# Kernel tuning notes

Hardware: AMD Instinct MI355X
Metric: run time of the kernel (lower is better)

The kernel has to match this reference:

```python
import jax, jax.numpy as jnp
import numpy as np

THRESHOLD = 0.9
DECAY = 0.6


def setup_inputs() -> dict:
    key = jax.random.key(0)
    k1, k2, k3 = jax.random.split(key, 3)
    T, B, I, H, O = 100, 256, 784, 1024, 10
    # binary-ish spike input (rand fill, thresholded to emulate Poisson spikes)
    x = (jax.random.uniform(k1, (T, B, I)) < 0.3).astype(jnp.float32)
    W1 = 0.01 * jax.random.normal(k2, (I, H), dtype=jnp.float32)
    W2 = 0.01 * jax.random.normal(k3, (H, O), dtype=jnp.float32)
    return {"input_spikes_time": x, "W1": W1, "W2": W2}


def reference(input_spikes_time, W1, W2):
    T, B, _ = input_spikes_time.shape
    H = W1.shape[1]
    O = W2.shape[1]
    dt = input_spikes_time.dtype

    def lif(mem, current):
        # mem = mem*decay + I; spike if mem >= threshold; soft reset
        mem = mem * DECAY + current
        spikes = (mem >= THRESHOLD).astype(dt)
        mem = mem - spikes * THRESHOLD
        return mem, spikes

    def step(carry, x_t):
        mem1, mem2 = carry
        hidden_u = x_t @ W1                 # [B, H]
        mem1, hidden_spikes = lif(mem1, hidden_u)
        output_u = hidden_spikes @ W2       # [B, O]
        mem2, output_spikes = lif(mem2, output_u)
        return (mem1, mem2), (hidden_spikes, output_spikes)

    init = (jnp.zeros((B, H), dt), jnp.zeros((B, O), dt))
    _, (hidden_all, output_all) = jax.lax.scan(step, init, input_spikes_time)
    return hidden_all, output_all
```

## Files before the change

kernel.cpp:

```cpp
#include <hip/hip_runtime.h>
#include <hip/hip_bf16.h>

#define T_STEPS 100
#define BATCH   256
#define IN_DIM  784
#define HID_DIM 1024
#define OUT_DIM 10
#define M_ROWS  (T_STEPS * BATCH)
#define KPAD    800
#define NT      25
#define STG     12288
#define DECAY   0.6f
#define THRESH  0.9f

typedef __attribute__((ext_vector_type(8))) short bf16x8;
typedef __attribute__((ext_vector_type(4))) float f32x4;

#define PACK8(dstp, v0, v1)                                                                        \
    {                                                                                              \
        unsigned int p0 = __builtin_amdgcn_perm(__builtin_bit_cast(unsigned int, (v0).y),          \
                                                __builtin_bit_cast(unsigned int, (v0).x), 0x07060302u); \
        unsigned int p1 = __builtin_amdgcn_perm(__builtin_bit_cast(unsigned int, (v0).w),          \
                                                __builtin_bit_cast(unsigned int, (v0).z), 0x07060302u); \
        unsigned int p2 = __builtin_amdgcn_perm(__builtin_bit_cast(unsigned int, (v1).y),          \
                                                __builtin_bit_cast(unsigned int, (v1).x), 0x07060302u); \
        unsigned int p3 = __builtin_amdgcn_perm(__builtin_bit_cast(unsigned int, (v1).w),          \
                                                __builtin_bit_cast(unsigned int, (v1).z), 0x07060302u); \
        *(uint4*)(dstp) = make_uint4(p0, p1, p2, p3);                                              \
    }

#define GLL(g, l)                                                                                  \
    __builtin_amdgcn_global_load_lds((const __attribute__((address_space(1))) void*)(g),           \
                                     (__attribute__((address_space(3))) void*)(l), 16, 0, 0)

__device__ __forceinline__ void w1_split_body(const float* __restrict__ W1,
                                              unsigned short* __restrict__ Th,
                                              unsigned short* __restrict__ Tl,
                                              int b2, int t,
                                              unsigned short lh[32][33],
                                              unsigned short ll[32][33]) {
    const int nb = (b2 & 31) * 32;
    const int kb = (b2 >> 5) * 32;
    const int ln = t & 31, lk = t >> 5;
    #pragma unroll
    for (int i = 0; i < 4; ++i) {
        const int k = kb + lk + i * 8;
        const float w = (k < IN_DIM) ? W1[(size_t)k * HID_DIM + nb + ln] : 0.f;
        __hip_bfloat16 h = __float2bfloat16(w);
        float hf = __bfloat162float(h);
        __hip_bfloat16 l = __float2bfloat16(w - hf);
        lh[lk + i * 8][ln] = __builtin_bit_cast(unsigned short, h);
        ll[lk + i * 8][ln] = __builtin_bit_cast(unsigned short, l);
    }
    __syncthreads();
    const int o_n = t >> 3;
    const int o_k = (t & 7) * 4;
    ushort4 vh, vl;
    vh.x = lh[o_k + 0][o_n]; vh.y = lh[o_k + 1][o_n];
    vh.z = lh[o_k + 2][o_n]; vh.w = lh[o_k + 3][o_n];
    vl.x = ll[o_k + 0][o_n]; vl.y = ll[o_k + 1][o_n];
    vl.z = ll[o_k + 2][o_n]; vl.w = ll[o_k + 3][o_n];
    *(ushort4*)&Th[(size_t)(nb + o_n) * KPAD + kb + o_k] = vh;
    *(ushort4*)&Tl[(size_t)(nb + o_n) * KPAD + kb + o_k] = vl;
}

__global__ __launch_bounds__(256) void prep(const float* __restrict__ X,
                                            const float* __restrict__ W1,
                                            unsigned short* __restrict__ Xb,
                                            unsigned short* __restrict__ Th,
                                            unsigned short* __restrict__ Tl,
                                            float* __restrict__ outu) {
    __shared__ unsigned short lh[32][33];
    __shared__ unsigned short ll[32][33];
    const int bid = blockIdx.x;
    const int t   = threadIdx.x;

    if (bid < 10000) {
        const int gid = bid * 256 + t;
        const int r   = gid / 100;
        const int c   = gid - r * 100;
        unsigned short* dst = Xb + (size_t)r * KPAD + c * 8;
        if (c < 98) {
            const float* s = X + (size_t)r * IN_DIM + c * 8;
            float4 v0 = *(const float4*)s, v1 = *(const float4*)(s + 4);
            PACK8(dst, v0, v1);
        } else {
            *(uint4*)dst = make_uint4(0u, 0u, 0u, 0u);
        }
    } else if (bid < 10800) {
        w1_split_body(W1, Th, Tl, bid - 10000, t, lh, ll);
    } else {
        float4* p = (float4*)outu;
        p[(bid - 10800) * 256 + t] = make_float4(0.f, 0.f, 0.f, 0.f);
    }
}

__global__ __launch_bounds__(256) void prep_small(const float* __restrict__ W1,
                                                  unsigned short* __restrict__ Th,
                                                  unsigned short* __restrict__ Tl,
                                                  float* __restrict__ outu) {
    __shared__ unsigned short lh[32][33];
    __shared__ unsigned short ll[32][33];
    const int bid = blockIdx.x;
    const int t   = threadIdx.x;
    if (bid < 800) {
        w1_split_body(W1, Th, Tl, bid, t, lh, ll);
    } else {
        float4* p = (float4*)outu;
        p[(bid - 800) * 256 + t] = make_float4(0.f, 0.f, 0.f, 0.f);
    }
}

__global__ __launch_bounds__(256, 3) void gemm1_pipe2(const unsigned short* __restrict__ Xb,
                                                      const unsigned short* __restrict__ Th,
                                                      const unsigned short* __restrict__ Tl,
                                                      float* __restrict__ C) {
    __shared__ unsigned short smem[2 * STG];

    const int tid = threadIdx.x;
    const int bid = blockIdx.x;
    const int xcd = bid & 7;
    const int j_  = bid >> 3;
    const int m0  = (xcd * 25 + (j_ >> 3)) * 128;
    const int n0  = (j_ & 7) * 128;

    const int lane = tid & 63, wv = tid >> 6;
    const int wm   = (wv & 1) * 64, wn = (wv >> 1) * 64;
    const int ml   = lane & 15, quad = lane >> 4;

    const int row  = tid >> 2;
    const int slot = tid & 3;
    const int sOff = (slot ^ ((row >> 1) & 3)) * 8;

    const unsigned short* gA0 = Xb + (size_t)(m0 + row)      * KPAD + sOff;
    const unsigned short* gA1 = Xb + (size_t)(m0 + row + 64) * KPAD + sOff;
    const unsigned short* gH0 = Th + (size_t)(n0 + row)      * KPAD + sOff;
    const unsigned short* gH1 = Th + (size_t)(n0 + row + 64) * KPAD + sOff;
    const unsigned short* gL0 = Tl + (size_t)(n0 + row)      * KPAD + sOff;
    const unsigned short* gL1 = Tl + (size_t)(n0 + row + 64) * KPAD + sOff;

#define STAGE(bf, it)                                                     \
    {                                                                     \
        unsigned short* b_ = smem + (bf) * STG;                           \
        const int k_ = (it) * 32;                                         \
        GLL(gA0 + k_, b_ + tid * 8);                                      \
        GLL(gA1 + k_, b_ + 2048 + tid * 8);                               \
        GLL(gH0 + k_, b_ + 4096 + tid * 8);                               \
        GLL(gH1 + k_, b_ + 6144 + tid * 8);                               \
        GLL(gL0 + k_, b_ + 8192 + tid * 8);                               \
        GLL(gL1 + k_, b_ + 10240 + tid * 8);                              \
    }

    f32x4 acc[4][4];
    #pragma unroll
    for (int i = 0; i < 4; ++i)
        #pragma unroll
        for (int j = 0; j < 4; ++j)
            acc[i][j] = (f32x4){0.f, 0.f, 0.f, 0.f};

    int offA[4], offB[4];
    #pragma unroll
    for (int i = 0; i < 4; ++i) {
        const int m = wm + i * 16 + ml;
        offA[i] = m * 32 + ((quad ^ ((m >> 1) & 3)) * 8);
    }
    #pragma unroll
    for (int j = 0; j < 4; ++j) {
        const int n = wn + j * 16 + ml;
        offB[j] = n * 32 + ((quad ^ ((n >> 1) & 3)) * 8);
    }

    STAGE(0, 0);

    int buf = 0;
    for (int it = 0; it < NT; ++it) {
        asm volatile("s_waitcnt vmcnt(0)" ::: "memory");
        __builtin_amdgcn_s_barrier();
        asm volatile("" ::: "memory");

        if (it + 1 < NT) STAGE(buf ^ 1, it + 1);

        const unsigned short* base = smem + buf * STG;
        bf16x8 af[4], bh[4], bl[4];
        #pragma unroll
        for (int i = 0; i < 4; ++i)
            af[i] = *(const bf16x8*)&base[offA[i]];
        #pragma unroll
        for (int j = 0; j < 4; ++j) {
            bh[j] = *(const bf16x8*)&base[4096 + offB[j]];
            bl[j] = *(const bf16x8*)&base[8192 + offB[j]];
        }

        __builtin_amdgcn_s_setprio(1);
        #pragma unroll
        for (int i = 0; i < 4; ++i)
            #pragma unroll
            for (int j = 0; j < 4; ++j) {
                acc[i][j] = __builtin_amdgcn_mfma_f32_16x16x32_bf16(af[i], bh[j], acc[i][j], 0, 0, 0);
                acc[i][j] = __builtin_amdgcn_mfma_f32_16x16x32_bf16(af[i], bl[j], acc[i][j], 0, 0, 0);
            }
        __builtin_amdgcn_s_setprio(0);

        buf ^= 1;
    }
#undef STAGE

    #pragma unroll
    for (int i = 0; i < 4; ++i)
        #pragma unroll
        for (int j = 0; j < 4; ++j) {
            const int r0 = m0 + wm + i * 16 + quad * 4;
            const int c0 = n0 + wn + j * 16 + ml;
            #pragma unroll
            for (int r = 0; r < 4; ++r)
                C[(size_t)(r0 + r) * HID_DIM + c0] = acc[i][j][r];
        }
}

__global__ __launch_bounds__(256, 3) void gemm1_fallback(const float* __restrict__ X,
                                                         const unsigned short* __restrict__ Th,
                                                         const unsigned short* __restrict__ Tl,
                                                         float* __restrict__ C) {
    __shared__ unsigned short As[128 * 32];
    __shared__ unsigned short Bhs[128 * 32];
    __shared__ unsigned short Bls[128 * 32];

    const int tid = threadIdx.x;
    const int bid = blockIdx.x;
    const int xcd = bid & 7;
    const int j_  = bid >> 3;
    const int m0  = (xcd * 25 + (j_ >> 3)) * 128;
    const int n0  = (j_ & 7) * 128;

    const int lane = tid & 63, wv = tid >> 6;
    const int wm   = (wv & 1) * 64, wn = (wv >> 1) * 64;
    const int ml   = lane & 15, quad = lane >> 4;

    const int sr = tid >> 2;
    const int sc = tid & 3;
    const int f0 = (sr >> 1) & 3;
    const int w0 = sr * 32 + ((sc ^ f0) * 8);
    const int w1 = (sr + 64) * 32 + ((sc ^ f0) * 8);

    const float*          Xa = X  + (size_t)(m0 + sr)      * IN_DIM + sc * 8;
    const float*          Xc = X  + (size_t)(m0 + sr + 64) * IN_DIM + sc * 8;
    const unsigned short* Ha = Th + (size_t)(n0 + sr)      * KPAD   + sc * 8;
    const unsigned short* Hb = Th + (size_t)(n0 + sr + 64) * KPAD   + sc * 8;
    const unsigned short* La = Tl + (size_t)(n0 + sr)      * KPAD   + sc * 8;
    const unsigned short* Lb = Tl + (size_t)(n0 + sr + 64) * KPAD   + sc * 8;

    f32x4 acc[4][4];
    #pragma unroll
    for (int i = 0; i < 4; ++i)
        #pragma unroll
        for (int j = 0; j < 4; ++j)
            acc[i][j] = (f32x4){0.f, 0.f, 0.f, 0.f};

    float4 xa0 = *(const float4*)&Xa[0], xa1 = *(const float4*)&Xa[4];
    float4 xb0 = *(const float4*)&Xc[0], xb1 = *(const float4*)&Xc[4];
    uint4  vh0 = *(const uint4*)&Ha[0],  vh1 = *(const uint4*)&Hb[0];
    uint4  vl0 = *(const uint4*)&La[0],  vl1 = *(const uint4*)&Lb[0];
    PACK8(&As[w0], xa0, xa1);
    PACK8(&As[w1], xb0, xb1);
    *(uint4*)&Bhs[w0] = vh0;  *(uint4*)&Bhs[w1] = vh1;
    *(uint4*)&Bls[w0] = vl0;  *(uint4*)&Bls[w1] = vl1;
    __syncthreads();

    for (int it = 0; it < NT; ++it) {
        bf16x8 af[4], bh[4], bl[4];
        #pragma unroll
        for (int i = 0; i < 4; ++i) {
            const int m = wm + i * 16 + ml;
            af[i] = *(const bf16x8*)&As[m * 32 + ((quad ^ ((m >> 1) & 3)) * 8)];
        }
        #pragma unroll
        for (int j = 0; j < 4; ++j) {
            const int n   = wn + j * 16 + ml;
            const int idx = n * 32 + ((quad ^ ((n >> 1) & 3)) * 8);
            bh[j] = *(const bf16x8*)&Bhs[idx];
            bl[j] = *(const bf16x8*)&Bls[idx];
        }

        const bool have_next = (it + 1 < NT);
        if (have_next) {
            const int kt = (it + 1) * 32;
            const int c0 = kt + sc * 8;
            const bool v0 = (c0 < IN_DIM), v1 = (c0 + 4 < IN_DIM);
            xa0 = v0 ? *(const float4*)&Xa[kt]     : make_float4(0.f, 0.f, 0.f, 0.f);
            xa1 = v1 ? *(const float4*)&Xa[kt + 4] : make_float4(0.f, 0.f, 0.f, 0.f);
            xb0 = v0 ? *(const float4*)&Xc[kt]     : make_float4(0.f, 0.f, 0.f, 0.f);
            xb1 = v1 ? *(const float4*)&Xc[kt + 4] : make_float4(0.f, 0.f, 0.f, 0.f);
            vh0 = *(const uint4*)&Ha[kt];  vh1 = *(const uint4*)&Hb[kt];
            vl0 = *(const uint4*)&La[kt];  vl1 = *(const uint4*)&Lb[kt];
        }

        #pragma unroll
        for (int i = 0; i < 4; ++i)
            #pragma unroll
            for (int j = 0; j < 4; ++j) {
                acc[i][j] = __builtin_amdgcn_mfma_f32_16x16x32_bf16(af[i], bh[j], acc[i][j], 0, 0, 0);
                acc[i][j] = __builtin_amdgcn_mfma_f32_16x16x32_bf16(af[i], bl[j], acc[i][j], 0, 0, 0);
            }

        __syncthreads();
        if (have_next) {
            PACK8(&As[w0], xa0, xa1);
            PACK8(&As[w1], xb0, xb1);
            *(uint4*)&Bhs[w0] = vh0;  *(uint4*)&Bhs[w1] = vh1;
            *(uint4*)&Bls[w0] = vl0;  *(uint4*)&Bls[w1] = vl1;
            __syncthreads();
        }
    }

    #pragma unroll
    for (int i = 0; i < 4; ++i)
        #pragma unroll
        for (int j = 0; j < 4; ++j) {
            const int r0 = m0 + wm + i * 16 + quad * 4;
            const int c0 = n0 + wn + j * 16 + ml;
            #pragma unroll
            for (int r = 0; r < 4; ++r)
                C[(size_t)(r0 + r) * HID_DIM + c0] = acc[i][j][r];
        }
}

__global__ __launch_bounds__(256) void lif1_fused(float* __restrict__ hid,
                                                  const float* __restrict__ W2,
                                                  float* __restrict__ outu) {
    const int idx = blockIdx.x * blockDim.x + threadIdx.x;
    const int stride = BATCH * HID_DIM;
    const int b  = idx >> 10;
    const int h0 = idx & 1023;

    float mem = 0.f;
    float u[10];
    #pragma unroll
    for (int c = 0; c < 10; ++c) u[c] = hid[(size_t)c * stride + idx];

    for (int t = 0; t < T_STEPS; t += 10) {
        float nu[10];
        if (t + 10 < T_STEPS) {
            #pragma unroll
            for (int c = 0; c < 10; ++c) nu[c] = hid[(size_t)(t + 10 + c) * stride + idx];
        }
        #pragma unroll
        for (int c = 0; c < 10; ++c) {
            mem = mem * DECAY + u[c];
            float s = (mem >= THRESH) ? 1.f : 0.f;
            mem -= s * THRESH;
            hid[(size_t)(t + c) * stride + idx] = s;
            if (s != 0.f) {
                float* od = outu + (size_t)(t + c) * (BATCH * OUT_DIM) + b * OUT_DIM;
                const float* w = W2 + (size_t)h0 * OUT_DIM;
                #pragma unroll
                for (int o = 0; o < OUT_DIM; ++o) atomicAdd(&od[o], w[o]);
            }
        }
        #pragma unroll
        for (int c = 0; c < 10; ++c) u[c] = nu[c];
    }
}

__global__ __launch_bounds__(256) void lif2(float* __restrict__ outp) {
    const int n = blockIdx.x * blockDim.x + threadIdx.x;
    const int stride = BATCH * OUT_DIM;
    if (n >= stride) return;
    float mem = 0.f;
    float u[10];
    #pragma unroll
    for (int c = 0; c < 10; ++c) u[c] = outp[(size_t)c * stride + n];
    for (int t = 0; t < T_STEPS; t += 10) {
        float nu[10];
        if (t + 10 < T_STEPS) {
            #pragma unroll
            for (int c = 0; c < 10; ++c) nu[c] = outp[(size_t)(t + 10 + c) * stride + n];
        }
        #pragma unroll
        for (int c = 0; c < 10; ++c) {
            mem = mem * DECAY + u[c];
            float s = (mem >= THRESH) ? 1.f : 0.f;
            mem -= s * THRESH;
            outp[(size_t)(t + c) * stride + n] = s;
        }
        #pragma unroll
        for (int c = 0; c < 10; ++c) u[c] = nu[c];
    }
}

extern "C" void kernel_launch(void* const* d_in, const int* in_sizes, int n_in,
                              void* d_out, int out_size, void* d_ws, size_t ws_size,
                              hipStream_t stream) {
    const float* x  = (const float*)d_in[0];
    const float* W1 = (const float*)d_in[1];
    const float* W2 = (const float*)d_in[2];
    float* out  = (float*)d_out;
    float* hid  = out;
    float* outu = out + (size_t)M_ROWS * HID_DIM;

    unsigned short* Th = (unsigned short*)d_ws;
    unsigned short* Tl = Th + (size_t)HID_DIM * KPAD;
    unsigned short* Xb = Tl + (size_t)HID_DIM * KPAD;

    const size_t ws_needed_big =
        (size_t)2 * HID_DIM * KPAD * sizeof(unsigned short) +
        (size_t)M_ROWS * KPAD * sizeof(unsigned short);

    if (ws_size >= ws_needed_big) {
        prep<<<11050, 256, 0, stream>>>(x, W1, Xb, Th, Tl, outu);
        gemm1_pipe2<<<1600, 256, 0, stream>>>(Xb, Th, Tl, hid);
    } else {
        prep_small<<<1050, 256, 0, stream>>>(W1, Th, Tl, outu);
        gemm1_fallback<<<1600, 256, 0, stream>>>(x, Th, Tl, hid);
    }

    lif1_fused<<<(BATCH * HID_DIM) / 256, 256, 0, stream>>>(hid, W2, outu);

    lif2<<<(BATCH * OUT_DIM + 255) / 256, 256, 0, stream>>>(outu);
}
```

Before: 277.2 us.

## Fuse lif2 into lif1 via last-block counter and coarsen prep X conversion

Removes the separate lif2 kernel launch. The last 10 blocks to finish lif1_fused, found through an atomic completion counter, spin until all blocks are done and then run the output-layer LIF scan. The prep kernel also processes four X chunks per thread, cutting its grid from 11050 to 3550 blocks. The counter lives in the workspace and is reset in prep. The spin-wait depends on every lif1 block eventually completing, which holds because the last 10 blocks only wait after all others have incremented the counter.

```diff
diff --git a/kernel.cpp b/kernel.cpp
--- a/kernel.cpp
+++ b/kernel.cpp
@@ -10,6 +10,7 @@
 #define KPAD    800
 #define NT      25
 #define STG     12288
+#define NBLK1   1024
 #define DECAY   0.6f
 #define THRESH  0.9f
 
@@ -69,36 +70,42 @@
                                             unsigned short* __restrict__ Xb,
                                             unsigned short* __restrict__ Th,
                                             unsigned short* __restrict__ Tl,
-                                            float* __restrict__ outu) {
+                                            float* __restrict__ outu,
+                                            unsigned int* __restrict__ ctr) {
     __shared__ unsigned short lh[32][33];
     __shared__ unsigned short ll[32][33];
     const int bid = blockIdx.x;
     const int t   = threadIdx.x;
 
-    if (bid < 10000) {
-        const int gid = bid * 256 + t;
-        const int r   = gid / 100;
-        const int c   = gid - r * 100;
-        unsigned short* dst = Xb + (size_t)r * KPAD + c * 8;
-        if (c < 98) {
-            const float* s = X + (size_t)r * IN_DIM + c * 8;
-            float4 v0 = *(const float4*)s, v1 = *(const float4*)(s + 4);
-            PACK8(dst, v0, v1);
-        } else {
-            *(uint4*)dst = make_uint4(0u, 0u, 0u, 0u);
-        }
-    } else if (bid < 10800) {
-        w1_split_body(W1, Th, Tl, bid - 10000, t, lh, ll);
+    if (bid < 2500) {
+        #pragma unroll
+        for (int i = 0; i < 4; ++i) {
+            const int gid = (bid * 256 + t) + i * 640000;
+            const int r   = gid / 100;
+            const int c   = gid - r * 100;
+            unsigned short* dst = Xb + (size_t)r * KPAD + c * 8;
+            if (c < 98) {
+                const float* s = X + (size_t)r * IN_DIM + c * 8;
+                float4 v0 = *(const float4*)s, v1 = *(const float4*)(s + 4);
+                PACK8(dst, v0, v1);
+            } else {
+                *(uint4*)dst = make_uint4(0u, 0u, 0u, 0u);
+            }
+        }
+    } else if (bid < 3300) {
+        w1_split_body(W1, Th, Tl, bid - 2500, t, lh, ll);
     } else {
+        if (bid == 3300 && t == 0) *ctr = 0u;
         float4* p = (float4*)outu;
-        p[(bid - 10800) * 256 + t] = make_float4(0.f, 0.f, 0.f, 0.f);
+        p[(bid - 3300) * 256 + t] = make_float4(0.f, 0.f, 0.f, 0.f);
     }
 }
 
 __global__ __launch_bounds__(256) void prep_small(const float* __restrict__ W1,
                                                   unsigned short* __restrict__ Th,
                                                   unsigned short* __restrict__ Tl,
-                                                  float* __restrict__ outu) {
+                                                  float* __restrict__ outu,
+                                                  unsigned int* __restrict__ ctr) {
     __shared__ unsigned short lh[32][33];
     __shared__ unsigned short ll[32][33];
     const int bid = blockIdx.x;
@@ -106,6 +113,7 @@
     if (bid < 800) {
         w1_split_body(W1, Th, Tl, bid, t, lh, ll);
     } else {
+        if (bid == 800 && t == 0) *ctr = 0u;
         float4* p = (float4*)outu;
         p[(bid - 800) * 256 + t] = make_float4(0.f, 0.f, 0.f, 0.f);
     }
@@ -326,7 +334,8 @@
 
 __global__ __launch_bounds__(256) void lif1_fused(float* __restrict__ hid,
                                                   const float* __restrict__ W2,
-                                                  float* __restrict__ outu) {
+                                                  float* __restrict__ outu,
+                                                  unsigned int* __restrict__ ctr) {
     const int idx = blockIdx.x * blockDim.x + threadIdx.x;
     const int stride = BATCH * HID_DIM;
     const int b  = idx >> 10;
@@ -359,31 +368,42 @@
         #pragma unroll
         for (int c = 0; c < 10; ++c) u[c] = nu[c];
     }
-}
-
-__global__ __launch_bounds__(256) void lif2(float* __restrict__ outp) {
-    const int n = blockIdx.x * blockDim.x + threadIdx.x;
-    const int stride = BATCH * OUT_DIM;
-    if (n >= stride) return;
-    float mem = 0.f;
-    float u[10];
-    #pragma unroll
-    for (int c = 0; c < 10; ++c) u[c] = outp[(size_t)c * stride + n];
+
+    __shared__ unsigned int s_old;
+    __threadfence();
+    __syncthreads();
+    if (threadIdx.x == 0) s_old = atomicAdd(ctr, 1u);
+    __syncthreads();
+    const unsigned int old = s_old;
+    if (old < (unsigned)(NBLK1 - 10)) return;
+
+    if (threadIdx.x == 0) {
+        while (atomicAdd(ctr, 0u) < (unsigned)NBLK1) __builtin_amdgcn_s_sleep(8);
+    }
+    __syncthreads();
+    __threadfence();
+
+    const int n = (int)(old - (unsigned)(NBLK1 - 10)) * 256 + (int)threadIdx.x;
+    const int ostride = BATCH * OUT_DIM;
+    float m2 = 0.f;
+    float v[10];
+    #pragma unroll
+    for (int c = 0; c < 10; ++c) v[c] = outu[(size_t)c * ostride + n];
     for (int t = 0; t < T_STEPS; t += 10) {
-        float nu[10];
+        float nv[10];
         if (t + 10 < T_STEPS) {
             #pragma unroll
-            for (int c = 0; c < 10; ++c) nu[c] = outp[(size_t)(t + 10 + c) * stride + n];
+            for (int c = 0; c < 10; ++c) nv[c] = outu[(size_t)(t + 10 + c) * ostride + n];
         }
         #pragma unroll
         for (int c = 0; c < 10; ++c) {
-            mem = mem * DECAY + u[c];
-            float s = (mem >= THRESH) ? 1.f : 0.f;
-            mem -= s * THRESH;
-            outp[(size_t)(t + c) * stride + n] = s;
-        }
-        #pragma unroll
-        for (int c = 0; c < 10; ++c) u[c] = nu[c];
+            m2 = m2 * DECAY + v[c];
+            float s = (m2 >= THRESH) ? 1.f : 0.f;
+            m2 -= s * THRESH;
+            outu[(size_t)(t + c) * ostride + n] = s;
+        }
+        #pragma unroll
+        for (int c = 0; c < 10; ++c) v[c] = nv[c];
     }
 }
 
@@ -397,23 +417,22 @@
     float* hid  = out;
     float* outu = out + (size_t)M_ROWS * HID_DIM;
 
-    unsigned short* Th = (unsigned short*)d_ws;
-    unsigned short* Tl = Th + (size_t)HID_DIM * KPAD;
-    unsigned short* Xb = Tl + (size_t)HID_DIM * KPAD;
+    unsigned short* Th  = (unsigned short*)d_ws;
+    unsigned short* Tl  = Th + (size_t)HID_DIM * KPAD;
+    unsigned int*   ctr = (unsigned int*)(Tl + (size_t)HID_DIM * KPAD);
+    unsigned short* Xb  = (unsigned short*)(ctr + 8);
 
     const size_t ws_needed_big =
-        (size_t)2 * HID_DIM * KPAD * sizeof(unsigned short) +
+        (size_t)2 * HID_DIM * KPAD * sizeof(unsigned short) + 32 +
         (size_t)M_ROWS * KPAD * sizeof(unsigned short);
 
     if (ws_size >= ws_needed_big) {
-        prep<<<11050, 256, 0, stream>>>(x, W1, Xb, Th, Tl, outu);
+        prep<<<3550, 256, 0, stream>>>(x, W1, Xb, Th, Tl, outu, ctr);
         gemm1_pipe2<<<1600, 256, 0, stream>>>(Xb, Th, Tl, hid);
     } else {
-        prep_small<<<1050, 256, 0, stream>>>(W1, Th, Tl, outu);
+        prep_small<<<1050, 256, 0, stream>>>(W1, Th, Tl, outu, ctr);
         gemm1_fallback<<<1600, 256, 0, stream>>>(x, Th, Tl, hid);
     }
 
-    lif1_fused<<<(BATCH * HID_DIM) / 256, 256, 0, stream>>>(hid, W2, outu);
-
-    lif2<<<(BATCH * OUT_DIM + 255) / 256, 256, 0, stream>>>(outu);
-}
+    lif1_fused<<<NBLK1, 256, 0, stream>>>(hid, W2, outu, ctr);
+}
```

New measurement: 428.8 us. +54.7%, slower.
